# Performance work log

Hardware: AMD Instinct MI355X
Metric: run time of the kernel (lower is better)

Reference implementation:

```python
import jax, jax.numpy as jnp
import numpy as np

VOCAB = 40
CHAR_EMB = 32
CELLS = [512, 1024, 2048]
EMB_SIZE = 512


def _gru_cell(x, h, w_ih, w_hh, b_ih, b_hh):
    # torch GRUCell: gates ordered (r, z, n); w_ih: [3H, In], w_hh: [3H, H]
    gi = x @ w_ih.T + b_ih
    gh = h @ w_hh.T + b_hh
    i_r, i_z, i_n = jnp.split(gi, 3, axis=-1)
    h_r, h_z, h_n = jnp.split(gh, 3, axis=-1)
    r = jax.nn.sigmoid(i_r + h_r)
    zg = jax.nn.sigmoid(i_z + h_z)
    n = jnp.tanh(i_n + r * h_n)
    return (1.0 - zg) * n + zg * h


def setup_inputs() -> dict:
    key = jax.random.key(0)
    ks = iter(jax.random.split(key, 32))

    def glorot(k, shape):
        fan = sum(shape)
        return jax.random.normal(k, shape, jnp.float32) * (2.0 / fan) ** 0.5

    inp = {
        "z": jax.random.normal(next(ks), (64, EMB_SIZE), jnp.float32),
        "emb": glorot(next(ks), (VOCAB, CHAR_EMB)),
        "fc_init_w": glorot(next(ks), (sum(CELLS), EMB_SIZE)),
        "fc_init_b": jnp.zeros((sum(CELLS),), jnp.float32),
        "fc_out_w": glorot(next(ks), (VOCAB, CELLS[-1])),
    }
    in_size = CHAR_EMB
    for li, h in enumerate(CELLS):
        inp[f"w_ih{li}"] = glorot(next(ks), (3 * h, in_size))
        inp[f"w_hh{li}"] = glorot(next(ks), (3 * h, h))
        inp[f"b_ih{li}"] = jnp.zeros((3 * h,), jnp.float32)
        inp[f"b_hh{li}"] = jnp.zeros((3 * h,), jnp.float32)
        in_size = h
    inp["max_len"] = 64
    inp["start_token"] = 1
    return inp


def reference(z, emb, fc_init_w, fc_init_b, fc_out_w,
              w_ih0, w_hh0, b_ih0, b_hh0,
              w_ih1, w_hh1, b_ih1, b_hh1,
              w_ih2, w_hh2, b_ih2, b_hh2,
              max_len, start_token):
    batch = z.shape[0]
    init_states = z @ fc_init_w.T + fc_init_b  # [B, sum(CELLS)]
    splits = np.cumsum(CELLS)[:-1].tolist()
    h0, h1, h2 = jnp.split(init_states, splits, axis=1)
    layers = [(w_ih0, w_hh0, b_ih0, b_hh0),
              (w_ih1, w_hh1, b_ih1, b_hh1),
              (w_ih2, w_hh2, b_ih2, b_hh2)]
    dec0 = jnp.full((batch,), start_token, dtype=jnp.int32)

    def step(carry, _):
        (h0, h1, h2), dec_in = carry
        x = emb[dec_in]  # [B, CHAR_EMB]
        hs = []
        for hprev, (wi, wh, bi, bh) in zip((h0, h1, h2), layers):
            hnew = _gru_cell(x, hprev, wi, wh, bi, bh)
            hs.append(hnew)
            x = hnew
        logits = x @ fc_out_w.T  # [B, VOCAB]
        dec = jnp.argmax(logits, axis=-1).astype(jnp.int32)
        return ((hs[0], hs[1], hs[2]), dec), dec

    _, toks = jax.lax.scan(step, ((h0, h1, h2), dec0), None, length=max_len)
    # toks: [max_len, B] -> [B, max_len, 1] to match torch stack of unsqueezed outputs
    return toks.T[:, :, None].astype(jnp.int64)
```

## Files before the change

### kernel.cpp

```cpp
#include <hip/hip_runtime.h>
#include <math.h>


#define BATCH 64

typedef short bf16x8 __attribute__((ext_vector_type(8)));
typedef float f32x4  __attribute__((ext_vector_type(4)));

__device__ __forceinline__ float sigmoid_f(float x) { return 1.0f / (1.0f + expf(-x)); }

__device__ __forceinline__ void fma4(float& a, const float4 w, const float4 x) {
    a = fmaf(w.x, x.x, a); a = fmaf(w.y, x.y, a);
    a = fmaf(w.z, x.z, a); a = fmaf(w.w, x.w, a);
}

__device__ __forceinline__ unsigned short f2bf(float x) {
    unsigned u = __float_as_uint(x);
    return (unsigned short)((u + 0x7fff + ((u >> 16) & 1)) >> 16);
}
__device__ __forceinline__ float bf2f(unsigned short h) {
    return __uint_as_float(((unsigned)h) << 16);
}
__device__ __forceinline__ void split_bf(float v, short& hi, short& lo) {
    unsigned short h = f2bf(v);
    hi = (short)h;
    lo = (short)f2bf(v - bf2f(h));
}

__device__ __forceinline__ void frag_scatter(short* xhi, short* xlo,
                                             int j, int b, float v) {
    short h, l2; split_bf(v, h, l2);
    const int kblk = j >> 5, off = j & 31;
    const int lp = ((off >> 3) << 4) + (b & 15);
    const int ii = off & 7;
    const int nt = b >> 4;
    const size_t idx = (((size_t)kblk * 4 + nt) * 64 + lp) * 8 + ii;
    xhi[idx] = h; xlo[idx] = l2;
}

__global__ __launch_bounds__(256) void init_misc(
    const float* __restrict__ z, float* __restrict__ zT4,
    int* __restrict__ dec, const int* __restrict__ start_tok)
{
    int tid = blockIdx.x * 256 + threadIdx.x;
    int b  = tid >> 7;
    int k4 = tid & 127;
    ((float4*)zT4)[k4 * 64 + b] = ((const float4*)z)[b * 128 + k4];
    if (tid < BATCH) dec[tid] = start_tok[0];
}

__global__ __launch_bounds__(256) void init_hstate(
    const float* __restrict__ zT4, const float* __restrict__ w,
    const float* __restrict__ bias,
    float* __restrict__ h0, float* __restrict__ h1, float* __restrict__ h2)
{
    const int wave = threadIdx.x >> 6;
    const int b    = threadIdx.x & 63;
    const int r    = blockIdx.x * 4 + wave;
    const float4* w4 = (const float4*)(w + (size_t)r * 512);
    const float4* z4 = (const float4*)zT4;
    float acc = 0.f;
#pragma unroll 8
    for (int k = 0; k < 128; ++k) fma4(acc, w4[k], z4[k * 64 + b]);
    acc += bias[r];
    float* dst; int j;
    if (r < 512)       { dst = h0; j = r; }
    else if (r < 1536) { dst = h1; j = r - 512; }
    else               { dst = h2; j = r - 1536; }
    dst[(((j >> 2) * 64 + b) << 2) + (j & 3)] = acc;
}

__global__ __launch_bounds__(256) void initfrag(
    const float* __restrict__ hT4, short* __restrict__ xhi, short* __restrict__ xlo)
{
    const int gid = blockIdx.x * 256 + threadIdx.x;
    const int j = gid >> 6, b = gid & 63;
    const float v = hT4[(((j >> 2) * 64 + b) << 2) + (j & 3)];
    frag_scatter(xhi, xlo, j, b, v);
}

template<int H, int IN>
__device__ __forceinline__ void wtransform_body(
    const float* __restrict__ w_ih, const float* __restrict__ w_hh,
    short* __restrict__ dhi, short* __restrict__ dlo)
{
    constexpr int KB = (IN + H) / 32;
    const int unit = blockIdx.x * 4 + (threadIdx.x >> 6);
    const int l    = threadIdx.x & 63;
    const int mtile = unit / KB, kblk = unit % KB;
    const int row = mtile * 16 + (l & 15);
    const int kk  = kblk * 32 + ((l >> 4) << 3);
    const float* src = (kk < IN) ? (w_ih + (size_t)row * IN + kk)
                                 : (w_hh + (size_t)row * H + (kk - IN));
    const float4 v0 = *(const float4*)src;
    const float4 v1 = *(const float4*)(src + 4);
    const float vv[8] = {v0.x, v0.y, v0.z, v0.w, v1.x, v1.y, v1.z, v1.w};
    short hi[8], lo[8];
#pragma unroll
    for (int i = 0; i < 8; ++i) split_bf(vv[i], hi[i], lo[i]);
    const size_t base = ((size_t)unit * 64 + l) * 8;
    *(bf16x8*)(dhi + base) = *(const bf16x8*)hi;
    *(bf16x8*)(dlo + base) = *(const bf16x8*)lo;
}
__global__ __launch_bounds__(256) void wtrans_l1(
    const float* __restrict__ a, const float* __restrict__ b,
    short* __restrict__ c, short* __restrict__ d)
{ wtransform_body<1024, 512>(a, b, c, d); }
__global__ __launch_bounds__(256) void wtrans_l2(
    const float* __restrict__ a, const float* __restrict__ b,
    short* __restrict__ c, short* __restrict__ d)
{ wtransform_body<2048, 1024>(a, b, c, d); }

__device__ __forceinline__ void mm_pipe(
    const short* __restrict__ wh, const short* __restrict__ wl,
    const short* __restrict__ bh, const short* __restrict__ bl,
    int k0, int k1, f32x4& accA, f32x4& accB)
{
    bf16x8 a0h,a0l,b0h,b0l,a1h,a1l,b1h,b1l,a2h,a2l,b2h,b2l,a3h,a3l,b3h,b3l;
#define LDST(KB_, AH,AL,BH,BL) \
    AH = *(const bf16x8*)(wh + (size_t)(KB_)*512); \
    AL = *(const bf16x8*)(wl + (size_t)(KB_)*512); \
    BH = *(const bf16x8*)(bh + (size_t)(KB_)*2048); \
    BL = *(const bf16x8*)(bl + (size_t)(KB_)*2048);
#define CONS(AH,AL,BH,BL) \
    accA = __builtin_amdgcn_mfma_f32_16x16x32_bf16(AH, BH, accA, 0,0,0); \
    accB = __builtin_amdgcn_mfma_f32_16x16x32_bf16(AH, BL, accB, 0,0,0); \
    accB = __builtin_amdgcn_mfma_f32_16x16x32_bf16(AL, BH, accB, 0,0,0);

    LDST(k0+0, a0h,a0l,b0h,b0l)
    LDST(k0+1, a1h,a1l,b1h,b1l)
    LDST(k0+2, a2h,a2l,b2h,b2l)
    LDST(k0+3, a3h,a3l,b3h,b3l)
    int kb = k0 + 4;
    for (; kb + 4 <= k1; kb += 4) {
        CONS(a0h,a0l,b0h,b0l) LDST(kb+0, a0h,a0l,b0h,b0l)
        CONS(a1h,a1l,b1h,b1l) LDST(kb+1, a1h,a1l,b1h,b1l)
        CONS(a2h,a2l,b2h,b2l) LDST(kb+2, a2h,a2l,b2h,b2l)
        CONS(a3h,a3l,b3h,b3l) LDST(kb+3, a3h,a3l,b3h,b3l)
    }
    CONS(a0h,a0l,b0h,b0l)
    CONS(a1h,a1l,b1h,b1l)
    CONS(a2h,a2l,b2h,b2l)
    CONS(a3h,a3l,b3h,b3l)
#undef LDST
#undef CONS
}

template<int H, int IN>
__device__ __forceinline__ void mfma_gate_body(
    const short* __restrict__ Whi, const short* __restrict__ Wlo,
    const short* __restrict__ XxHi, const short* __restrict__ XxLo,
    const short* __restrict__ XhHi, const short* __restrict__ XhLo,
    float* __restrict__ G)
{
    constexpr int KB  = (IN + H) / 32;
    constexpr int KXB = IN / 32;
    constexpr int KB2 = KB / 2;
    constexpr int GS  = H / 16;
    constexpr int KHR = KB - KXB;
    constexpr int KH0 = KB2 - KXB;

    __shared__ float red[4][4][64];

    const int tid = threadIdx.x;
    const int wid = tid >> 6;
    const int l   = tid & 63;
    const int nt  = wid & 3;
    const int kh  = wid >> 2;
    const int g   = blockIdx.x / GS;
    const int jb  = blockIdx.x % GS;

    const size_t abase = ((size_t)(g * GS + jb) * KB) * 512 + (size_t)l * 8;
    const short* wh = Whi + abase;
    const short* wl = Wlo + abase;
    const size_t bofs = (size_t)nt * 512 + (size_t)l * 8;

    f32x4 aXa = {0,0,0,0}, aXb = {0,0,0,0}, aHa = {0,0,0,0}, aHb = {0,0,0,0};

    if (kh == 0) {
        mm_pipe(wh, wl, XxHi + bofs, XxLo + bofs, 0, KXB, aXa, aXb);
        mm_pipe(wh + (size_t)KXB * 512, wl + (size_t)KXB * 512,
                XhHi + bofs, XhLo + bofs, 0, KH0, aHa, aHb);
    } else {
        mm_pipe(wh + (size_t)KXB * 512, wl + (size_t)KXB * 512,
                XhHi + bofs, XhLo + bofs, KH0, KHR, aHa, aHb);
    }

    float SX[4], SH[4];
#pragma unroll
    for (int t = 0; t < 4; ++t) { SX[t] = aXa[t] + aXb[t]; SH[t] = aHa[t] + aHb[t]; }

    if (kh == 1) {
#pragma unroll
        for (int t = 0; t < 4; ++t) red[nt][t][l] = SH[t];
    }
    __syncthreads();
    if (kh == 0) {
        const int b = nt * 16 + (l & 15);
#pragma unroll
        for (int t = 0; t < 4; ++t) {
            SH[t] += red[nt][t][l];
            const int j = jb * 16 + ((l >> 4) << 2) + t;
            if (g == 0)      G[(size_t)(0 * H + j) * 64 + b] = SX[t] + SH[t];
            else if (g == 1) G[(size_t)(1 * H + j) * 64 + b] = SX[t] + SH[t];
            else {
                G[(size_t)(2 * H + j) * 64 + b] = SX[t];
                G[(size_t)(3 * H + j) * 64 + b] = SH[t];
            }
        }
    }
}
__global__ __launch_bounds__(512, 2) void mfma_l1(
    const short* __restrict__ a, const short* __restrict__ b,
    const short* __restrict__ c, const short* __restrict__ d,
    const short* __restrict__ e, const short* __restrict__ f,
    float* __restrict__ g)
{ mfma_gate_body<1024, 512>(a, b, c, d, e, f, g); }
__global__ __launch_bounds__(512, 2) void mfma_l2(
    const short* __restrict__ a, const short* __restrict__ b,
    const short* __restrict__ c, const short* __restrict__ d,
    const short* __restrict__ e, const short* __restrict__ f,
    float* __restrict__ g)
{ mfma_gate_body<2048, 1024>(a, b, c, d, e, f, g); }

template<int H>
__device__ __forceinline__ void comb_body(
    const float* __restrict__ G,
    const float* __restrict__ b_ih, const float* __restrict__ b_hh,
    float* __restrict__ hT4, short* __restrict__ xhi, short* __restrict__ xlo)
{
    const int gid = blockIdx.x * 256 + threadIdx.x;
    const int j = gid >> 6, b = gid & 63;
    const float R  = G[(size_t)(0 * H + j) * 64 + b];
    const float Z  = G[(size_t)(1 * H + j) * 64 + b];
    const float NX = G[(size_t)(2 * H + j) * 64 + b];
    const float NH = G[(size_t)(3 * H + j) * 64 + b];
    const float r  = sigmoid_f(R + b_ih[j] + b_hh[j]);
    const float zg = sigmoid_f(Z + b_ih[H + j] + b_hh[H + j]);
    const float n  = tanhf(NX + b_ih[2 * H + j] + r * (NH + b_hh[2 * H + j]));
    const int idx = (((j >> 2) * 64 + b) << 2) + (j & 3);
    const float hp = hT4[idx];
    const float hn = (1.f - zg) * n + zg * hp;
    hT4[idx] = hn;
    frag_scatter(xhi, xlo, j, b, hn);
}
__global__ __launch_bounds__(256) void comb_l1(
    const float* __restrict__ G, const float* __restrict__ bi,
    const float* __restrict__ bh, float* __restrict__ h,
    short* __restrict__ xh, short* __restrict__ xl)
{ comb_body<1024>(G, bi, bh, h, xh, xl); }
__global__ __launch_bounds__(256) void comb_l2(
    const float* __restrict__ G, const float* __restrict__ bi,
    const float* __restrict__ bh, float* __restrict__ h,
    short* __restrict__ xh, short* __restrict__ xl)
{ comb_body<2048>(G, bi, bh, h, xh, xl); }

template<int IN, int H, int C, bool L0>
__device__ __forceinline__ void gru2_body(
    const float* __restrict__ xT4,
    const float* __restrict__ emb, const int* __restrict__ dec,
    const float* __restrict__ hT4_in, float* __restrict__ hT4_out,
    const float* __restrict__ w_ih, const float* __restrict__ w_hh,
    const float* __restrict__ b_ih, const float* __restrict__ b_hh,
    short* __restrict__ xw_hi, short* __restrict__ xw_lo)
{
    constexpr int Q  = (IN + H) / 4;
    constexpr int QX = IN / 4;
    constexpr int QW = Q / 8;

    const int tid  = threadIdx.x;
    const int wave = tid >> 6;
    const int b    = tid & 63;
    const int j0   = blockIdx.x * C;
    const int q0 = wave * QW;
    const int q1 = q0 + QW;

    float accR[C], accZ[C], accNX[C], accNH[C];
#pragma unroll
    for (int c = 0; c < C; ++c) { accR[c]=0.f; accZ[c]=0.f; accNX[c]=0.f; accNH[c]=0.f; }

    {
        const int xe = (q1 < QX) ? q1 : QX;
        if (q0 < xe) {
            const float4* xsrc;
            if (L0) { xsrc = (const float4*)(emb + dec[b] * 32); }
            else    { xsrc = (const float4*)xT4; }
            for (int q = q0; q < xe; ++q) {
                const float4 x = L0 ? xsrc[q] : xsrc[q * 64 + b];
#pragma unroll
                for (int c = 0; c < C; ++c) {
                    const int j = j0 + c;
                    fma4(accR[c],  *(const float4*)(w_ih + ((size_t)j * IN) + 4*q), x);
                    fma4(accZ[c],  *(const float4*)(w_ih + ((size_t)(j + H) * IN) + 4*q), x);
                    fma4(accNX[c], *(const float4*)(w_ih + ((size_t)(j + 2*H) * IN) + 4*q), x);
                }
            }
        }
    }
    {
        const int hs0 = (q0 > QX) ? q0 : QX;
        if (hs0 < q1) {
            const float4* h4 = (const float4*)hT4_in;
#pragma unroll 2
            for (int q = hs0; q < q1; ++q) {
                const int qh = q - QX;
                const float4 hv = h4[qh * 64 + b];
#pragma unroll
                for (int c = 0; c < C; ++c) {
                    const int j = j0 + c;
                    fma4(accR[c],  *(const float4*)(w_hh + ((size_t)j * H) + 4*qh), hv);
                    fma4(accZ[c],  *(const float4*)(w_hh + ((size_t)(j + H) * H) + 4*qh), hv);
                    fma4(accNH[c], *(const float4*)(w_hh + ((size_t)(j + 2*H) * H) + 4*qh), hv);
                }
            }
        }
    }

    __shared__ float red[8][C][4][64];
#pragma unroll
    for (int c = 0; c < C; ++c) {
        red[wave][c][0][b] = accR[c];
        red[wave][c][1][b] = accZ[c];
        red[wave][c][2][b] = accNX[c];
        red[wave][c][3][b] = accNH[c];
    }
    __syncthreads();

    if (tid < C * 64) {
        const int c  = tid >> 6;
        const int bb = tid & 63;
        float R = 0.f, Z = 0.f, NX = 0.f, NH = 0.f;
#pragma unroll
        for (int w = 0; w < 8; ++w) {
            R += red[w][c][0][bb]; Z += red[w][c][1][bb];
            NX += red[w][c][2][bb]; NH += red[w][c][3][bb];
        }
        const int j = j0 + c;
        const float r  = sigmoid_f(R + b_ih[j]     + b_hh[j]);
        const float zg = sigmoid_f(Z + b_ih[j + H] + b_hh[j + H]);
        const float n  = tanhf(NX + b_ih[j + 2 * H] + r * (NH + b_hh[j + 2 * H]));
        const float hp = hT4_in[(((j >> 2) * 64 + bb) << 2) + (j & 3)];
        const float hn = (1.f - zg) * n + zg * hp;
        hT4_out[(((j >> 2) * 64 + bb) << 2) + (j & 3)] = hn;
        if (xw_hi) frag_scatter(xw_hi, xw_lo, j, bb, hn);
    }
}
__global__ __launch_bounds__(512) void gru_l0(
    const float* __restrict__ emb, const int* __restrict__ dec,
    const float* __restrict__ hin, float* __restrict__ hout,
    const float* __restrict__ wi, const float* __restrict__ wh,
    const float* __restrict__ bi, const float* __restrict__ bh,
    short* __restrict__ xh, short* __restrict__ xl)
{ gru2_body<32, 512, 2, true>(nullptr, emb, dec, hin, hout, wi, wh, bi, bh, xh, xl); }
__global__ __launch_bounds__(512) void gru_fb1(
    const float* __restrict__ x, const float* __restrict__ hin, float* __restrict__ hout,
    const float* __restrict__ wi, const float* __restrict__ wh,
    const float* __restrict__ bi, const float* __restrict__ bh)
{ gru2_body<512, 1024, 4, false>(x, nullptr, nullptr, hin, hout, wi, wh, bi, bh, nullptr, nullptr); }
__global__ __launch_bounds__(512) void gru_fb2(
    const float* __restrict__ x, const float* __restrict__ hin, float* __restrict__ hout,
    const float* __restrict__ wi, const float* __restrict__ wh,
    const float* __restrict__ bi, const float* __restrict__ bh)
{ gru2_body<1024, 2048, 4, false>(x, nullptr, nullptr, hin, hout, wi, wh, bi, bh, nullptr, nullptr); }

__global__ __launch_bounds__(512) void out_k(
    const float* __restrict__ h2T4, const float* __restrict__ w_out,
    int* __restrict__ dec, int* __restrict__ out, int s, int max_len)
{
    __shared__ float hs[2048];
    __shared__ float lg[40];
    const int b    = blockIdx.x;
    const int tid  = threadIdx.x;
    const int wave = tid >> 6;
    const int lane = tid & 63;

    const float4* h4 = (const float4*)h2T4;
    ((float4*)hs)[tid] = h4[tid * 64 + b];
    __syncthreads();

    const float4* hs4 = (const float4*)hs;
#pragma unroll
    for (int v = wave * 5; v < wave * 5 + 5; ++v) {
        const float4* w4 = (const float4*)(w_out + (size_t)v * 2048);
        float acc = 0.f;
#pragma unroll
        for (int it = 0; it < 8; ++it) {
            const int k4 = it * 64 + lane;
            fma4(acc, w4[k4], hs4[k4]);
        }
#pragma unroll
        for (int off = 32; off > 0; off >>= 1)
            acc += __shfl_down(acc, off, 64);
        if (lane == 0) lg[v] = acc;
    }
    __syncthreads();

    if (tid == 0) {
        float best = lg[0];
        int bi = 0;
#pragma unroll
        for (int v = 1; v < 40; ++v) {
            const float val = lg[v];
            if (val > best) { best = val; bi = v; }
        }
        dec[b] = bi;
        out[b * max_len + s] = bi;
    }
}

extern "C" void kernel_launch(void* const* d_in, const int* in_sizes, int n_in,
                              void* d_out, int out_size, void* d_ws, size_t ws_size,
                              hipStream_t stream)
{
    const float* z         = (const float*)d_in[0];
    const float* emb       = (const float*)d_in[1];
    const float* fc_init_w = (const float*)d_in[2];
    const float* fc_init_b = (const float*)d_in[3];
    const float* fc_out_w  = (const float*)d_in[4];
    const float* w_ih0 = (const float*)d_in[5];
    const float* w_hh0 = (const float*)d_in[6];
    const float* b_ih0 = (const float*)d_in[7];
    const float* b_hh0 = (const float*)d_in[8];
    const float* w_ih1 = (const float*)d_in[9];
    const float* w_hh1 = (const float*)d_in[10];
    const float* b_ih1 = (const float*)d_in[11];
    const float* b_hh1 = (const float*)d_in[12];
    const float* w_ih2 = (const float*)d_in[13];
    const float* w_hh2 = (const float*)d_in[14];
    const float* b_ih2 = (const float*)d_in[15];
    const float* b_hh2 = (const float*)d_in[16];
    const int* start_tok = (const int*)d_in[18];

    int* out = (int*)d_out;
    const int max_len = out_size / BATCH;
    char* ws = (char*)d_ws;

    const size_t NEED = 100401408;

    if (ws_size >= NEED) {
        short* Wf1hi = (short*)(ws + 0);
        short* Wf1lo = (short*)(ws + 9437184);
        short* Wf2hi = (short*)(ws + 18874368);
        short* Wf2lo = (short*)(ws + 56623104);
        short* XB0hi = (short*)(ws + 94371840);
        short* XB0lo = (short*)(ws + 94437376);
        short* XB1hi[2] = { (short*)(ws + 94502912), (short*)(ws + 94765056) };
        short* XB1lo[2] = { (short*)(ws + 94633984), (short*)(ws + 94896128) };
        short* XB2hi[2] = { (short*)(ws + 95027200), (short*)(ws + 95551488) };
        short* XB2lo[2] = { (short*)(ws + 95289344), (short*)(ws + 95813632) };
        float* h0a = (float*)(ws + 96075776);
        float* h0b = (float*)(ws + 96206848);
        float* h1  = (float*)(ws + 96337920);
        float* h2  = (float*)(ws + 96600064);
        float* zT4 = (float*)(ws + 97124352);
        float* G1  = (float*)(ws + 97255424);
        float* G2  = (float*)(ws + 98304000);
        int*   dec = (int*)  (ws + 100401152);

        wtrans_l1<<<2304, 256, 0, stream>>>(w_ih1, w_hh1, Wf1hi, Wf1lo);
        wtrans_l2<<<9216, 256, 0, stream>>>(w_ih2, w_hh2, Wf2hi, Wf2lo);
        init_misc<<<32, 256, 0, stream>>>(z, zT4, dec, start_tok);
        init_hstate<<<896, 256, 0, stream>>>(zT4, fc_init_w, fc_init_b, h0a, h1, h2);
        initfrag<<<256, 256, 0, stream>>>(h1, XB1hi[0], XB1lo[0]);
        initfrag<<<512, 256, 0, stream>>>(h2, XB2hi[0], XB2lo[0]);

        for (int s = 0; s < max_len; ++s) {
            const int pi = s & 1, po = pi ^ 1;
            const float* h0i = pi ? h0b : h0a;
            float*       h0o = pi ? h0a : h0b;
            gru_l0<<<256, 512, 0, stream>>>(emb, dec, h0i, h0o,
                                            w_ih0, w_hh0, b_ih0, b_hh0,
                                            XB0hi, XB0lo);
            mfma_l1<<<192, 512, 0, stream>>>(Wf1hi, Wf1lo, XB0hi, XB0lo,
                                             XB1hi[pi], XB1lo[pi], G1);
            comb_l1<<<256, 256, 0, stream>>>(G1, b_ih1, b_hh1, h1,
                                             XB1hi[po], XB1lo[po]);
            mfma_l2<<<384, 512, 0, stream>>>(Wf2hi, Wf2lo, XB1hi[po], XB1lo[po],
                                             XB2hi[pi], XB2lo[pi], G2);
            comb_l2<<<512, 256, 0, stream>>>(G2, b_ih2, b_hh2, h2,
                                             XB2hi[po], XB2lo[po]);
            out_k<<<64, 512, 0, stream>>>(h2, fc_out_w, dec, out, s, max_len);
        }
    } else {
        float* zT4    = (float*)(ws + 0);
        float* h0b2[2] = { (float*)(ws + 131072), (float*)(ws + 262144) };
        float* h1b2[2] = { (float*)(ws + 393216), (float*)(ws + 655360) };
        float* h2b2[2] = { (float*)(ws + 917504), (float*)(ws + 1441792) };
        int*   dec    = (int*)(ws + 1966080);

        init_misc<<<32, 256, 0, stream>>>(z, zT4, dec, start_tok);
        init_hstate<<<896, 256, 0, stream>>>(zT4, fc_init_w, fc_init_b,
                                             h0b2[0], h1b2[0], h2b2[0]);
        for (int s = 0; s < max_len; ++s) {
            const int pi = s & 1, po = pi ^ 1;
            gru_l0<<<256, 512, 0, stream>>>(emb, dec, h0b2[pi], h0b2[po],
                                            w_ih0, w_hh0, b_ih0, b_hh0,
                                            nullptr, nullptr);
            gru_fb1<<<256, 512, 0, stream>>>(h0b2[po], h1b2[pi], h1b2[po],
                                             w_ih1, w_hh1, b_ih1, b_hh1);
            gru_fb2<<<512, 512, 0, stream>>>(h1b2[po], h2b2[pi], h2b2[po],
                                             w_ih2, w_hh2, b_ih2, b_hh2);
            out_k<<<64, 512, 0, stream>>>(h2b2[po], fc_out_w, dec, out, s, max_len);
        }
    }
}
```

Before: 3.961 ms.

## Split-K the MFMA gate GEMMs across two blocks and stage weights via LDS

Each gate-GEMM tile is now split along K across two blocks and two wave-halves, which doubles the grid for the layer-1 and layer-2 matmuls. Each block writes its own partial gate sums into a doubled G buffer, and the combine kernels add the two halves. Weight tiles are loaded asynchronously into double-buffered LDS with global_load_lds, followed by block-wide syncs. This adds G traffic and barriers per group in exchange for more parallelism on a latency-bound small-batch GEMV-like workload.

```diff
diff --git a/kernel.cpp b/kernel.cpp
--- a/kernel.cpp
+++ b/kernel.cpp
@@ -111,41 +111,6 @@
     short* __restrict__ c, short* __restrict__ d)
 { wtransform_body<2048, 1024>(a, b, c, d); }
 
-__device__ __forceinline__ void mm_pipe(
-    const short* __restrict__ wh, const short* __restrict__ wl,
-    const short* __restrict__ bh, const short* __restrict__ bl,
-    int k0, int k1, f32x4& accA, f32x4& accB)
-{
-    bf16x8 a0h,a0l,b0h,b0l,a1h,a1l,b1h,b1l,a2h,a2l,b2h,b2l,a3h,a3l,b3h,b3l;
-#define LDST(KB_, AH,AL,BH,BL) \
-    AH = *(const bf16x8*)(wh + (size_t)(KB_)*512); \
-    AL = *(const bf16x8*)(wl + (size_t)(KB_)*512); \
-    BH = *(const bf16x8*)(bh + (size_t)(KB_)*2048); \
-    BL = *(const bf16x8*)(bl + (size_t)(KB_)*2048);
-#define CONS(AH,AL,BH,BL) \
-    accA = __builtin_amdgcn_mfma_f32_16x16x32_bf16(AH, BH, accA, 0,0,0); \
-    accB = __builtin_amdgcn_mfma_f32_16x16x32_bf16(AH, BL, accB, 0,0,0); \
-    accB = __builtin_amdgcn_mfma_f32_16x16x32_bf16(AL, BH, accB, 0,0,0);
-
-    LDST(k0+0, a0h,a0l,b0h,b0l)
-    LDST(k0+1, a1h,a1l,b1h,b1l)
-    LDST(k0+2, a2h,a2l,b2h,b2l)
-    LDST(k0+3, a3h,a3l,b3h,b3l)
-    int kb = k0 + 4;
-    for (; kb + 4 <= k1; kb += 4) {
-        CONS(a0h,a0l,b0h,b0l) LDST(kb+0, a0h,a0l,b0h,b0l)
-        CONS(a1h,a1l,b1h,b1l) LDST(kb+1, a1h,a1l,b1h,b1l)
-        CONS(a2h,a2l,b2h,b2l) LDST(kb+2, a2h,a2l,b2h,b2l)
-        CONS(a3h,a3l,b3h,b3l) LDST(kb+3, a3h,a3l,b3h,b3l)
-    }
-    CONS(a0h,a0l,b0h,b0l)
-    CONS(a1h,a1l,b1h,b1l)
-    CONS(a2h,a2l,b2h,b2l)
-    CONS(a3h,a3l,b3h,b3l)
-#undef LDST
-#undef CONS
-}
-
 template<int H, int IN>
 __device__ __forceinline__ void mfma_gate_body(
     const short* __restrict__ Whi, const short* __restrict__ Wlo,
@@ -155,35 +120,71 @@
 {
     constexpr int KB  = (IN + H) / 32;
     constexpr int KXB = IN / 32;
-    constexpr int KB2 = KB / 2;
     constexpr int GS  = H / 16;
-    constexpr int KHR = KB - KXB;
-    constexpr int KH0 = KB2 - KXB;
-
-    __shared__ float red[4][4][64];
+    constexpr int KQ4 = KB / 4;
+    constexpr int NG  = KQ4 / 4;
+
+    __shared__ __align__(16) short Ast[2][2][4][2][512];
+    __shared__ float red[4][8][64];
 
     const int tid = threadIdx.x;
     const int wid = tid >> 6;
     const int l   = tid & 63;
     const int nt  = wid & 3;
     const int kh  = wid >> 2;
-    const int g   = blockIdx.x / GS;
-    const int jb  = blockIdx.x % GS;
-
-    const size_t abase = ((size_t)(g * GS + jb) * KB) * 512 + (size_t)l * 8;
-    const short* wh = Whi + abase;
-    const short* wl = Wlo + abase;
-    const size_t bofs = (size_t)nt * 512 + (size_t)l * 8;
+    const int kq   = blockIdx.x & 1;
+    const int rest = blockIdx.x >> 1;
+    const int g    = rest / GS;
+    const int jb   = rest % GS;
+
+    const int kbase = kq * (KB / 2) + kh * KQ4;
+    const size_t abase = ((size_t)(g * GS + jb) * KB) * 512;
+    const int pl  = nt & 1;
+    const int kl0 = nt >> 1;
+    const short* wsrc = (pl ? Wlo : Whi) + abase;
 
     f32x4 aXa = {0,0,0,0}, aXb = {0,0,0,0}, aHa = {0,0,0,0}, aHb = {0,0,0,0};
 
-    if (kh == 0) {
-        mm_pipe(wh, wl, XxHi + bofs, XxLo + bofs, 0, KXB, aXa, aXb);
-        mm_pipe(wh + (size_t)KXB * 512, wl + (size_t)KXB * 512,
-                XhHi + bofs, XhLo + bofs, 0, KH0, aHa, aHb);
-    } else {
-        mm_pipe(wh + (size_t)KXB * 512, wl + (size_t)KXB * 512,
-                XhHi + bofs, XhLo + bofs, KH0, KHR, aHa, aHb);
+    auto stage = [&](int buf, int grp) {
+        const int kbb = kbase + grp * 4;
+#pragma unroll
+        for (int u = 0; u < 2; ++u) {
+            const int kloc = kl0 + u * 2;
+            const short* ga = wsrc + (size_t)(kbb + kloc) * 512 + (size_t)l * 8;
+            __builtin_amdgcn_global_load_lds(
+                (const __attribute__((address_space(1))) unsigned int*)ga,
+                (__attribute__((address_space(3))) unsigned int*)&Ast[buf][kh][kloc][pl][0],
+                16, 0, 0);
+        }
+    };
+
+    auto comp = [&](int buf, const short* bsH, const short* bsL,
+                    f32x4& A1, f32x4& A2) {
+#pragma unroll
+        for (int i = 0; i < 4; ++i) {
+            const bf16x8 ah = *(const bf16x8*)&Ast[buf][kh][i][0][(size_t)l * 8];
+            const bf16x8 al = *(const bf16x8*)&Ast[buf][kh][i][1][(size_t)l * 8];
+            const bf16x8 bh = *(const bf16x8*)(bsH + (size_t)i * 2048 + (size_t)nt * 512 + (size_t)l * 8);
+            const bf16x8 bl = *(const bf16x8*)(bsL + (size_t)i * 2048 + (size_t)nt * 512 + (size_t)l * 8);
+            A1 = __builtin_amdgcn_mfma_f32_16x16x32_bf16(ah, bh, A1, 0, 0, 0);
+            A2 = __builtin_amdgcn_mfma_f32_16x16x32_bf16(ah, bl, A2, 0, 0, 0);
+            A2 = __builtin_amdgcn_mfma_f32_16x16x32_bf16(al, bh, A2, 0, 0, 0);
+        }
+    };
+
+    stage(0, 0);
+    __syncthreads();
+#pragma unroll
+    for (int grp = 0; grp < NG; ++grp) {
+        const int buf = grp & 1;
+        if (grp + 1 < NG) stage(buf ^ 1, grp + 1);
+        const int kbb = kbase + grp * 4;
+        if (kbb < KXB)
+            comp(buf, XxHi + (size_t)kbb * 2048, XxLo + (size_t)kbb * 2048, aXa, aXb);
+        else
+            comp(buf, XhHi + (size_t)(kbb - KXB) * 2048,
+                      XhLo + (size_t)(kbb - KXB) * 2048, aHa, aHb);
+        __syncthreads();
     }
 
     float SX[4], SH[4];
@@ -192,20 +193,24 @@
 
     if (kh == 1) {
 #pragma unroll
-        for (int t = 0; t < 4; ++t) red[nt][t][l] = SH[t];
+        for (int t = 0; t < 4; ++t) {
+            red[nt][t][l]     = SX[t];
+            red[nt][4 + t][l] = SH[t];
+        }
     }
     __syncthreads();
     if (kh == 0) {
         const int b = nt * 16 + (l & 15);
 #pragma unroll
         for (int t = 0; t < 4; ++t) {
-            SH[t] += red[nt][t][l];
+            SX[t] += red[nt][t][l];
+            SH[t] += red[nt][4 + t][l];
             const int j = jb * 16 + ((l >> 4) << 2) + t;
-            if (g == 0)      G[(size_t)(0 * H + j) * 64 + b] = SX[t] + SH[t];
-            else if (g == 1) G[(size_t)(1 * H + j) * 64 + b] = SX[t] + SH[t];
+            if (g == 0)      G[(size_t)((kq * 4 + 0) * H + j) * 64 + b] = SX[t] + SH[t];
+            else if (g == 1) G[(size_t)((kq * 4 + 1) * H + j) * 64 + b] = SX[t] + SH[t];
             else {
-                G[(size_t)(2 * H + j) * 64 + b] = SX[t];
-                G[(size_t)(3 * H + j) * 64 + b] = SH[t];
+                G[(size_t)((kq * 4 + 2) * H + j) * 64 + b] = SX[t];
+                G[(size_t)((kq * 4 + 3) * H + j) * 64 + b] = SH[t];
             }
         }
     }
@@ -231,10 +236,12 @@
 {
     const int gid = blockIdx.x * 256 + threadIdx.x;
     const int j = gid >> 6, b = gid & 63;
-    const float R  = G[(size_t)(0 * H + j) * 64 + b];
-    const float Z  = G[(size_t)(1 * H + j) * 64 + b];
-    const float NX = G[(size_t)(2 * H + j) * 64 + b];
-    const float NH = G[(size_t)(3 * H + j) * 64 + b];
+    const size_t o = (size_t)j * 64 + b;
+    const size_t P = (size_t)H * 64;
+    const float R  = G[0 * P + o] + G[4 * P + o];
+    const float Z  = G[1 * P + o] + G[5 * P + o];
+    const float NX = G[2 * P + o] + G[6 * P + o];
+    const float NH = G[3 * P + o] + G[7 * P + o];
     const float r  = sigmoid_f(R + b_ih[j] + b_hh[j]);
     const float zg = sigmoid_f(Z + b_ih[H + j] + b_hh[H + j]);
     const float n  = tanhf(NX + b_ih[2 * H + j] + r * (NH + b_hh[2 * H + j]));
@@ -435,7 +442,7 @@
     const int max_len = out_size / BATCH;
     char* ws = (char*)d_ws;
 
-    const size_t NEED = 100401408;
+    const size_t NEED = 103547136;
 
     if (ws_size >= NEED) {
         short* Wf1hi = (short*)(ws + 0);
@@ -454,8 +461,8 @@
         float* h2  = (float*)(ws + 96600064);
         float* zT4 = (float*)(ws + 97124352);
         float* G1  = (float*)(ws + 97255424);
-        float* G2  = (float*)(ws + 98304000);
-        int*   dec = (int*)  (ws + 100401152);
+        float* G2  = (float*)(ws + 99352576);
+        int*   dec = (int*)  (ws + 103546880);
 
         wtrans_l1<<<2304, 256, 0, stream>>>(w_ih1, w_hh1, Wf1hi, Wf1lo);
         wtrans_l2<<<9216, 256, 0, stream>>>(w_ih2, w_hh2, Wf2hi, Wf2lo);
@@ -471,11 +478,11 @@
             gru_l0<<<256, 512, 0, stream>>>(emb, dec, h0i, h0o,
                                             w_ih0, w_hh0, b_ih0, b_hh0,
                                             XB0hi, XB0lo);
-            mfma_l1<<<192, 512, 0, stream>>>(Wf1hi, Wf1lo, XB0hi, XB0lo,
+            mfma_l1<<<384, 512, 0, stream>>>(Wf1hi, Wf1lo, XB0hi, XB0lo,
                                              XB1hi[pi], XB1lo[pi], G1);
             comb_l1<<<256, 256, 0, stream>>>(G1, b_ih1, b_hh1, h1,
                                              XB1hi[po], XB1lo[po]);
-            mfma_l2<<<384, 512, 0, stream>>>(Wf2hi, Wf2lo, XB1hi[po], XB1lo[po],
+            mfma_l2<<<768, 512, 0, stream>>>(Wf2hi, Wf2lo, XB1hi[po], XB1lo[po],
                                              XB2hi[pi], XB2lo[pi], G2);
             comb_l2<<<512, 256, 0, stream>>>(G2, b_ih2, b_hh2, h2,
                                              XB2hi[po], XB2lo[po]);
```

Result: faster. 3.210 ms (-19.0%).
